# Kernel tuning notes

Measured on AMD Instinct MI355X. Metric: run time of the kernel, lower is better.

## Reference

```python
import jax, jax.numpy as jnp
import numpy as np


def _make_area_table():
    # Surrogate for create_table_neighbour_code_to_surface_area((1,1,1)):
    # a fixed 256-entry lookup that is exactly 0 for the all-empty (0) and
    # all-full (255) neighbour codes and strictly positive otherwise, which
    # preserves the structure the loss relies on (gt_surface = area > 0,
    # gt_foreground = code==255, gt_background = code==0).
    pop = np.array([bin(c).count("1") for c in range(256)], dtype=np.float32)
    return (0.5 * np.minimum(pop, 8.0 - pop)).astype(np.float32)


def _conv3d(x, w):
    # x: [B,1,D,H,W], w: [1,1,2,2,2], VALID 2x2x2 sliding window
    return jax.lax.conv_general_dilated(
        x, w, window_strides=(1, 1, 1), padding="VALID",
        dimension_numbers=("NCDHW", "OIDHW", "NCDHW"))


def setup_inputs() -> dict:
    key = jax.random.key(0)
    k1, k2 = jax.random.split(key)
    B, D, H, W = 2, 128, 256, 256
    preds = jax.random.normal(k1, (B, 1, D, H, W), dtype=jnp.float32)
    targets = jax.random.randint(k2, (B, 1, D, H, W), 0, 2).astype(jnp.float32)
    power = (2.0 ** jnp.arange(8, dtype=jnp.float32)).reshape(1, 1, 2, 2, 2)
    kernel = jnp.ones((1, 1, 2, 2, 2), dtype=jnp.float32)
    area = jnp.asarray(_make_area_table())
    return {"preds": preds, "targets": targets, "power": power,
            "kernel": kernel, "area": area}


def reference(preds, targets, power, kernel, area):
    eps = 1e-5
    bsz = preds.shape[0]

    # log-prob that all 8 voxels of each 2x2x2 cube are foreground / background
    fg = jnp.exp(_conv3d(jax.nn.log_sigmoid(preds), kernel)).reshape(bsz, -1)
    bg = jnp.exp(_conv3d(jax.nn.log_sigmoid(-preds), kernel)).reshape(bsz, -1)
    surf = 1.0 - fg - bg

    # neighbour codes from binary targets (no grad path)
    codes = jax.lax.stop_gradient(_conv3d(targets, power)).astype(jnp.int32).reshape(bsz, -1)
    gt_area = area[codes.reshape(-1)].reshape(bsz, -1)
    gt_fg = (codes == 255).astype(jnp.float32)
    gt_bg = (codes == 0).astype(jnp.float32)
    gt_surf = (gt_area > 0).astype(jnp.float32)

    fg_dice = (2.0 * jnp.sum(fg * gt_fg, -1) + eps) / (jnp.sum(fg, -1) + jnp.sum(gt_fg, -1) + eps)
    bg_dice = (2.0 * jnp.sum(bg * gt_bg, -1) + eps) / (jnp.sum(bg, -1) + jnp.sum(gt_bg, -1) + eps)
    surf_dice = (2.0 * jnp.sum(surf * gt_area, -1) + eps) / (jnp.sum((surf + gt_surf) * gt_area, -1) + eps)

    dice = (fg_dice + bg_dice + surf_dice) / 3.0
    return 1.0 - jnp.mean(dice)
```

## Files before the change

### kernel.cpp

```cpp
#include <hip/hip_runtime.h>

typedef float f2 __attribute__((ext_vector_type(2)));

#define DD 128
#define HH 256
#define WW 256
#define OD 127
#define SLICE_F (HH*WW)
#define CHUNK 16
#define TEN_B 3072
#define BUF_B 6144
#define NBUF 3
#define WAVE_B (NBUF*BUF_B)
#define AS1 __attribute__((address_space(1)))
#define AS3 __attribute__((address_space(3)))

#define VMCNT0()  asm volatile("s_waitcnt vmcnt(0)"  ::: "memory")
#define VMCNT6()  asm volatile("s_waitcnt vmcnt(6)"  ::: "memory")
#define VMCNT12() asm volatile("s_waitcnt vmcnt(12)" ::: "memory")

struct Sl { f2 uu2[4]; f2 vv2[4]; f2 ps[4]; };

__device__ __forceinline__ void stage_slice(const float* __restrict__ pB,
                                            const float* __restrict__ tB,
                                            int s, char* lb, int h0w, int lane)
{
    const size_t so = ((size_t)s << 16) + (size_t)(lane << 2);
    #pragma unroll
    for (int r = 0; r < 3; ++r) {
        const int grow = min(h0w + r, HH - 1);
        const float* gp = pB + so + ((size_t)grow << 8);
        const float* gt = tB + so + ((size_t)grow << 8);
        __builtin_amdgcn_global_load_lds((const AS1 void*)gp,
            (AS3 void*)(lb + r * 1024 + lane * 16), 16, 0, 0);
        __builtin_amdgcn_global_load_lds((const AS1 void*)gt,
            (AS3 void*)(lb + TEN_B + r * 1024 + lane * 16), 16, 0, 0);
    }
}

__device__ __forceinline__ void make_sl(const char* lb, int lane, Sl& S)
{
    const float* sp = (const float*)lb;
    const float* st = (const float*)(lb + TEN_B);
    const int co = lane << 2;
    const float4 p0 = *(const float4*)(sp + co);
    const float4 p1 = *(const float4*)(sp + co + 256);
    const float4 p2 = *(const float4*)(sp + co + 512);
    const float4 t0 = *(const float4*)(st + co);
    const float4 t1 = *(const float4*)(st + co + 256);
    const float4 t2 = *(const float4*)(st + co + 512);

    float u0x=__expf(p0.x), u0y=__expf(p0.y), u0z=__expf(p0.z), u0w=__expf(p0.w);
    float u1x=__expf(p1.x), u1y=__expf(p1.y), u1z=__expf(p1.z), u1w=__expf(p1.w);
    float u2x=__expf(p2.x), u2y=__expf(p2.y), u2z=__expf(p2.z), u2w=__expf(p2.w);

    f2 uA0 = {u0x,u1x}, uB0 = {u1x,u2x};
    f2 uA1 = {u0y,u1y}, uB1 = {u1y,u2y};
    f2 uA2 = {u0z,u1z}, uB2 = {u1z,u2z};
    f2 uA3 = {u0w,u1w}, uB3 = {u1w,u2w};

    f2 W0 = uA0*uB0, W1 = uA1*uB1, W2 = uA2*uB2, W3 = uA3*uB3;
    f2 Q0 = (uA0+1.f)*(uB0+1.f);
    f2 Q1 = (uA1+1.f)*(uB1+1.f);
    f2 Q2 = (uA2+1.f)*(uB2+1.f);
    f2 Q3 = (uA3+1.f)*(uB3+1.f);
    f2 W4, Q4;
    W4.x = __shfl_down(W0.x, 1); W4.y = __shfl_down(W0.y, 1);
    Q4.x = __shfl_down(Q0.x, 1); Q4.y = __shfl_down(Q0.y, 1);

    S.uu2[0]=W0*W1; S.uu2[1]=W1*W2; S.uu2[2]=W2*W3; S.uu2[3]=W3*W4;
    S.vv2[0]=Q0*Q1; S.vv2[1]=Q1*Q2; S.vv2[2]=Q2*Q3; S.vv2[3]=Q3*Q4;

    f2 cs0 = {t0.x+t1.x, t1.x+t2.x};
    f2 cs1 = {t0.y+t1.y, t1.y+t2.y};
    f2 cs2 = {t0.z+t1.z, t1.z+t2.z};
    f2 cs3 = {t0.w+t1.w, t1.w+t2.w};
    f2 cs4; cs4.x = __shfl_down(cs0.x, 1); cs4.y = __shfl_down(cs0.y, 1);
    S.ps[0]=cs0+cs1; S.ps[1]=cs1+cs2; S.ps[2]=cs2+cs3; S.ps[3]=cs3+cs4;
}

__device__ __forceinline__ void do_cubes(const Sl& P, const Sl& C,
        const f2 vAll, const f2 v3,
        f2& aFG, f2& aF255, f2& aBG, f2& aBG0, f2& aSFA,
        f2& c255, f2& c0, f2& cMN)
{
    #pragma unroll
    for (int j = 0; j < 4; ++j) {
        f2 E = P.uu2[j] * C.uu2[j];
        f2 Q = P.vv2[j] * C.vv2[j];
        f2 vj = (j == 3) ? v3 : vAll;
        f2 r; r.x = __builtin_amdgcn_rcpf(Q.x); r.y = __builtin_amdgcn_rcpf(Q.y);
        r *= vj;
        f2 fg = E * r;
        f2 pop = P.ps[j] + C.ps[j];
        f2 i255, i0, mn;
        i255.x = fmaxf(pop.x - 7.f, 0.f); i255.y = fmaxf(pop.y - 7.f, 0.f);
        i0.x   = fmaxf(1.f - pop.x, 0.f); i0.y   = fmaxf(1.f - pop.y, 0.f);
        mn.x   = 4.f - fabsf(pop.x - 4.f); mn.y = 4.f - fabsf(pop.y - 4.f);
        mn *= vj;
        aFG  += fg;
        aBG  += r;
        aF255 = fg * i255 + aF255;
        aBG0  = r  * i0   + aBG0;
        c255  = i255 * vj + c255;
        c0    = i0   * vj + c0;
        aSFA  = (fg + r) * mn + aSFA;
        cMN  += mn;
    }
}

#define LAYER(SRC, DST)                                                        \
    do {                                                                       \
        if (t + 3 <= NT) {                                                     \
            stage_slice(pB, tB, d0 + t + 3, wb + sw * BUF_B, h0w, lane);       \
            VMCNT12();               \
        } else if (t + 2 <= NT) {                                              \
            VMCNT6();                            \
        } else {                                                               \
            VMCNT0();                                                          \
        }                                                                      \
        __builtin_amdgcn_sched_barrier(0);                                     \
        make_sl(wb + sr * BUF_B, lane, DST);                                   \
        do_cubes(SRC, DST, vAll, v3, aFG, aF255, aBG, aBG0, aSFA, c255, c0, cMN); \
        sr = (sr + 1 == NBUF) ? 0 : sr + 1;                                    \
        sw = (sw + 1 == NBUF) ? 0 : sw + 1;                                    \
    } while (0)

__global__ __launch_bounds__(256, 2)
void loss_main(const float* __restrict__ preds,
               const float* __restrict__ targets,
               float* __restrict__ ws)
{
    __shared__ __align__(16) char smem[4 * WAVE_B];
    __shared__ float red[32];

    const int lane = threadIdx.x & 63;
    const int wv   = threadIdx.x >> 6;
    char* wb = smem + wv * WAVE_B;

    const int nid = ((blockIdx.x & 7) << 6) + (blockIdx.x >> 3);
    const int x = nid & 31;
    const int y = (nid >> 5) & 7;
    const int b = nid >> 8;

    const int h0w = (x << 3) + (wv << 1);
    const int d0  = y << 4;
    const int NT  = min(CHUNK, OD - d0);

    const float* pB = preds   + (size_t)b * DD * SLICE_F;
    const float* tB = targets + (size_t)b * DD * SLICE_F;

    const float rv1 = (h0w + 1 < HH - 1) ? 1.f : 0.f;
    const float v63 = (lane == 63) ? 0.f : 1.f;
    const f2 vAll = {1.f, rv1};
    const f2 v3   = {v63, v63 * rv1};

    f2 aFG={0,0}, aF255={0,0}, aBG={0,0}, aBG0={0,0}, aSFA={0,0};
    f2 c255={0,0}, c0={0,0}, cMN={0,0};

    stage_slice(pB, tB, d0,     wb,             h0w, lane);
    stage_slice(pB, tB, d0 + 1, wb + BUF_B,     h0w, lane);
    stage_slice(pB, tB, d0 + 2, wb + 2 * BUF_B, h0w, lane);
    VMCNT12();
    __builtin_amdgcn_sched_barrier(0);

    Sl A, B;
    make_sl(wb, lane, A);

    int sr = 1, sw = 0;
    int t = 0;
    for (;;) {
        LAYER(A, B);
        if (++t >= NT) break;
        LAYER(B, A);
        if (++t >= NT) break;
    }

    float acc[8] = {aFG.x+aFG.y, aF255.x+aF255.y, c255.x+c255.y,
                    aBG.x+aBG.y, aBG0.x+aBG0.y,   c0.x+c0.y,
                    aSFA.x+aSFA.y, cMN.x+cMN.y};
    #pragma unroll
    for (int i = 0; i < 8; ++i) {
        float v = acc[i];
        #pragma unroll
        for (int off = 32; off > 0; off >>= 1) v += __shfl_xor(v, off);
        acc[i] = v;
    }
    float mine = acc[0];
    mine = (lane == 1) ? acc[1] : mine;
    mine = (lane == 2) ? acc[2] : mine;
    mine = (lane == 3) ? acc[3] : mine;
    mine = (lane == 4) ? acc[4] : mine;
    mine = (lane == 5) ? acc[5] : mine;
    mine = (lane == 6) ? acc[6] : mine;
    mine = (lane == 7) ? acc[7] : mine;
    if (lane < 8) red[wv * 8 + lane] = mine;
    __syncthreads();
    if (wv == 0 && lane < 8)
        ws[nid * 8 + lane] = red[lane] + red[8 + lane] + red[16 + lane] + red[24 + lane];
}

__global__ void loss_final(const float* __restrict__ ws, float* __restrict__ out)
{
    __shared__ float part[16][17];
    __shared__ float S[16];
    const int tid = threadIdx.x;
    const int c = tid >> 4, sub = tid & 15;
    const int bb = c >> 3, s = c & 7;
    float v = 0.f;
    #pragma unroll 4
    for (int k = 0; k < 16; ++k) {
        int nid = bb * 256 + sub * 16 + k;
        v += ws[nid * 8 + s];
    }
    part[c][sub] = v;
    __syncthreads();
    if (tid < 16) {
        float q = 0.f;
        #pragma unroll
        for (int i = 0; i < 16; ++i) q += part[tid][i];
        S[tid] = q;
    }
    __syncthreads();
    if (tid == 0) {
        const float eps = 1e-5f;
        float dice = 0.f;
        #pragma unroll
        for (int b2 = 0; b2 < 2; ++b2) {
            const float* q = S + b2 * 8;
            float fg_dice = (2.f*q[1] + eps) / (q[0] + q[2] + eps);
            float bg_dice = (2.f*q[4] + eps) / (q[3] + q[5] + eps);
            float q6 = 0.5f * q[6];
            float q7 = 0.5f * q[7];
            float ss = q7 - q6;
            float sf_dice = (2.f*ss + eps) / (ss + q7 + eps);
            dice += fg_dice + bg_dice + sf_dice;
        }
        out[0] = 1.f - dice * (1.f/6.f);
    }
}

extern "C" void kernel_launch(void* const* d_in, const int* in_sizes, int n_in,
                              void* d_out, int out_size, void* d_ws, size_t ws_size,
                              hipStream_t stream)
{
    const float* preds   = (const float*)d_in[0];
    const float* targets = (const float*)d_in[1];
    float* ws = (float*)d_ws;

    loss_main<<<512, 256, 0, stream>>>(preds, targets, ws);
    loss_final<<<1, 256, 0, stream>>>(ws, (float*)d_out);
}
```

Before: 34.75 us.

## Share staged rows across waves in a block-wide LDS ring buffer

Each wave used to stage its own three rows (two rows plus a halo row) per slice, so overlapping halo rows were loaded twice across the four waves. Now the block cooperatively loads the nine unique rows of preds and targets into a shared four-slot ring, with loads spread across waves, and each wave reads its own row window from it. This cuts redundant global traffic by about a quarter but adds a block-wide barrier per layer, and relies on per-wave vmcnt values that differ by wave.

```diff
diff --git a/kernel.cpp b/kernel.cpp
--- a/kernel.cpp
+++ b/kernel.cpp
@@ -8,47 +8,50 @@
 #define OD 127
 #define SLICE_F (HH*WW)
 #define CHUNK 16
-#define TEN_B 3072
-#define BUF_B 6144
-#define NBUF 3
-#define WAVE_B (NBUF*BUF_B)
+#define TEN_B 9216
+#define SLOT_B 18432
+#define NBUF 4
 #define AS1 __attribute__((address_space(1)))
 #define AS3 __attribute__((address_space(3)))
 
-#define VMCNT0()  asm volatile("s_waitcnt vmcnt(0)"  ::: "memory")
-#define VMCNT6()  asm volatile("s_waitcnt vmcnt(6)"  ::: "memory")
-#define VMCNT12() asm volatile("s_waitcnt vmcnt(12)" ::: "memory")
+#define WAITP() do { if (wv < 2) asm volatile("s_waitcnt vmcnt(10)" ::: "memory"); \
+                     else        asm volatile("s_waitcnt vmcnt(8)"  ::: "memory"); } while (0)
+#define WAIT1() do { if (wv < 2) asm volatile("s_waitcnt vmcnt(5)"  ::: "memory"); \
+                     else        asm volatile("s_waitcnt vmcnt(4)"  ::: "memory"); } while (0)
+#define WAIT0() asm volatile("s_waitcnt vmcnt(0)" ::: "memory")
 
 struct Sl { f2 uu2[4]; f2 vv2[4]; f2 ps[4]; };
 
 __device__ __forceinline__ void stage_slice(const float* __restrict__ pB,
                                             const float* __restrict__ tB,
-                                            int s, char* lb, int h0w, int lane)
-{
-    const size_t so = ((size_t)s << 16) + (size_t)(lane << 2);
+                                            int s, char* lb, int h0, int wv, int lane)
+{
     #pragma unroll
-    for (int r = 0; r < 3; ++r) {
-        const int grow = min(h0w + r, HH - 1);
-        const float* gp = pB + so + ((size_t)grow << 8);
-        const float* gt = tB + so + ((size_t)grow << 8);
-        __builtin_amdgcn_global_load_lds((const AS1 void*)gp,
-            (AS3 void*)(lb + r * 1024 + lane * 16), 16, 0, 0);
-        __builtin_amdgcn_global_load_lds((const AS1 void*)gt,
-            (AS3 void*)(lb + TEN_B + r * 1024 + lane * 16), 16, 0, 0);
-    }
-}
-
-__device__ __forceinline__ void make_sl(const char* lb, int lane, Sl& S)
+    for (int i = 0; i < 5; ++i) {
+        const int L = i * 4 + wv;
+        if (L < 18) {
+            const int T = (L >= 9) ? 1 : 0;
+            const int r = L - T * 9;
+            const int grow = min(h0 + r, HH - 1);
+            const float* g = (T ? tB : pB)
+                           + ((size_t)s << 16) + ((size_t)grow << 8) + (lane << 2);
+            void* l = lb + T * TEN_B + r * 1024 + lane * 16;
+            __builtin_amdgcn_global_load_lds((const AS1 void*)g, (AS3 void*)l, 16, 0, 0);
+        }
+    }
+}
+
+__device__ __forceinline__ void make_sl(const char* lb, int wv, int lane, Sl& S)
 {
     const float* sp = (const float*)lb;
     const float* st = (const float*)(lb + TEN_B);
-    const int co = lane << 2;
-    const float4 p0 = *(const float4*)(sp + co);
-    const float4 p1 = *(const float4*)(sp + co + 256);
-    const float4 p2 = *(const float4*)(sp + co + 512);
-    const float4 t0 = *(const float4*)(st + co);
-    const float4 t1 = *(const float4*)(st + co + 256);
-    const float4 t2 = *(const float4*)(st + co + 512);
+    const int ro = ((wv << 1) << 8) + (lane << 2);
+    const float4 p0 = *(const float4*)(sp + ro);
+    const float4 p1 = *(const float4*)(sp + ro + 256);
+    const float4 p2 = *(const float4*)(sp + ro + 512);
+    const float4 t0 = *(const float4*)(st + ro);
+    const float4 t1 = *(const float4*)(st + ro + 256);
+    const float4 t2 = *(const float4*)(st + ro + 512);
 
     float u0x=__expf(p0.x), u0y=__expf(p0.y), u0z=__expf(p0.z), u0w=__expf(p0.w);
     float u1x=__expf(p1.x), u1y=__expf(p1.y), u1z=__expf(p1.z), u1w=__expf(p1.w);
@@ -112,18 +115,19 @@
 #define LAYER(SRC, DST)                                                        \
     do {                                                                       \
         if (t + 3 <= NT) {                                                     \
-            stage_slice(pB, tB, d0 + t + 3, wb + sw * BUF_B, h0w, lane);       \
-            VMCNT12();               \
+            stage_slice(pB, tB, d0 + t + 3, smem + sw * SLOT_B, h0, wv, lane); \
+            WAITP();         \
         } else if (t + 2 <= NT) {                                              \
-            VMCNT6();                            \
+            WAIT1();                                 \
         } else {                                                               \
-            VMCNT0();                                                          \
+            WAIT0();                                                           \
         }                                                                      \
+        __builtin_amdgcn_s_barrier();                                          \
         __builtin_amdgcn_sched_barrier(0);                                     \
-        make_sl(wb + sr * BUF_B, lane, DST);                                   \
+        make_sl(smem + sr * SLOT_B, wv, lane, DST);                            \
         do_cubes(SRC, DST, vAll, v3, aFG, aF255, aBG, aBG0, aSFA, c255, c0, cMN); \
-        sr = (sr + 1 == NBUF) ? 0 : sr + 1;                                    \
-        sw = (sw + 1 == NBUF) ? 0 : sw + 1;                                    \
+        sr = (sr + 1) & 3;                                                     \
+        sw = (sw + 1) & 3;                                                     \
     } while (0)
 
 __global__ __launch_bounds__(256, 2)
@@ -131,26 +135,26 @@
                const float* __restrict__ targets,
                float* __restrict__ ws)
 {
-    __shared__ __align__(16) char smem[4 * WAVE_B];
+    __shared__ __align__(16) char smem[NBUF * SLOT_B];
     __shared__ float red[32];
 
     const int lane = threadIdx.x & 63;
     const int wv   = threadIdx.x >> 6;
-    char* wb = smem + wv * WAVE_B;
 
     const int nid = ((blockIdx.x & 7) << 6) + (blockIdx.x >> 3);
     const int x = nid & 31;
     const int y = (nid >> 5) & 7;
     const int b = nid >> 8;
 
-    const int h0w = (x << 3) + (wv << 1);
-    const int d0  = y << 4;
-    const int NT  = min(CHUNK, OD - d0);
+    const int h0 = x << 3;
+    const int d0 = y << 4;
+    const int NT = min(CHUNK, OD - d0);
 
     const float* pB = preds   + (size_t)b * DD * SLICE_F;
     const float* tB = targets + (size_t)b * DD * SLICE_F;
 
-    const float rv1 = (h0w + 1 < HH - 1) ? 1.f : 0.f;
+    const int   myrow = h0 + (wv << 1);
+    const float rv1 = (myrow + 1 < HH - 1) ? 1.f : 0.f;
     const float v63 = (lane == 63) ? 0.f : 1.f;
     const f2 vAll = {1.f, rv1};
     const f2 v3   = {v63, v63 * rv1};
@@ -158,16 +162,17 @@
     f2 aFG={0,0}, aF255={0,0}, aBG={0,0}, aBG0={0,0}, aSFA={0,0};
     f2 c255={0,0}, c0={0,0}, cMN={0,0};
 
-    stage_slice(pB, tB, d0,     wb,             h0w, lane);
-    stage_slice(pB, tB, d0 + 1, wb + BUF_B,     h0w, lane);
-    stage_slice(pB, tB, d0 + 2, wb + 2 * BUF_B, h0w, lane);
-    VMCNT12();
+    stage_slice(pB, tB, d0,     smem,             h0, wv, lane);
+    stage_slice(pB, tB, d0 + 1, smem + SLOT_B,    h0, wv, lane);
+    stage_slice(pB, tB, d0 + 2, smem + 2*SLOT_B,  h0, wv, lane);
+    WAITP();
+    __builtin_amdgcn_s_barrier();
     __builtin_amdgcn_sched_barrier(0);
 
     Sl A, B;
-    make_sl(wb, lane, A);
-
-    int sr = 1, sw = 0;
+    make_sl(smem, wv, lane, A);
+
+    int sr = 1, sw = 3;
     int t = 0;
     for (;;) {
         LAYER(A, B);
```

After: 32.63 us, median of 2. -6.1%, faster.
